# Optimization experiments

Hardware: AMD Instinct MI355X
Metric: run time of the kernel (lower is better)

The kernel has to match this reference:

```python
import jax, jax.numpy as jnp
import numpy as np

N_NODES = 20000
N_EDGES = 320000
NUM_GRAPHS = 64
IN_DIM = 256


def setup_inputs() -> dict:
    key = jax.random.key(0)
    ks = jax.random.split(key, 12)
    x = jax.random.normal(ks[0], (N_NODES, IN_DIM), dtype=jnp.float32)
    edge_index = jax.random.randint(ks[1], (2, N_EDGES), 0, N_NODES, dtype=jnp.int64)
    batch = jnp.sort(jax.random.randint(ks[2], (N_NODES,), 0, NUM_GRAPHS, dtype=jnp.int64))
    def glorot(k, shape):
        lim = float(np.sqrt(6.0 / (shape[0] + shape[1])))
        return jax.random.uniform(k, shape, dtype=jnp.float32, minval=-lim, maxval=lim)
    W1 = glorot(ks[3], (IN_DIM, 256)); b1 = jnp.zeros((256,), jnp.float32)
    W2 = glorot(ks[4], (256, 128));   b2 = jnp.zeros((128,), jnp.float32)
    Wl1 = glorot(ks[5], (128, 64));   bl1 = jnp.zeros((64,), jnp.float32)
    Wl2 = glorot(ks[6], (64, 1));     bl2 = jnp.zeros((1,), jnp.float32)
    return {"x": x, "edge_index": edge_index, "batch": batch,
            "W1": W1, "b1": b1, "W2": W2, "b2": b2,
            "Wl1": Wl1, "bl1": bl1, "Wl2": Wl2, "bl2": bl2}


def gcn_conv(x, src, dst, W, b, n_nodes):
    # PyG GCNConv: add self-loops, symmetric normalization D^-1/2 (A+I) D^-1/2,
    # linear transform first, then gather-scale-scatter aggregation, then bias.
    loop = jnp.arange(n_nodes, dtype=src.dtype)
    s = jnp.concatenate([src, loop])
    d = jnp.concatenate([dst, loop])
    deg = jax.ops.segment_sum(jnp.ones_like(d, dtype=x.dtype), d, num_segments=n_nodes)
    dinv = jnp.where(deg > 0, jax.lax.rsqrt(deg), 0.0)
    norm = dinv[s] * dinv[d]                         # [E+N]
    h = x @ W                                        # [N, out]
    msg = h[s] * norm[:, None]                       # [E+N, out]
    out = jax.ops.segment_sum(msg, d, num_segments=n_nodes)
    return out + b


def global_mean_pool(x, batch, num_graphs):
    sums = jax.ops.segment_sum(x, batch, num_segments=num_graphs)
    cnts = jax.ops.segment_sum(jnp.ones((x.shape[0],), x.dtype), batch, num_segments=num_graphs)
    return sums / jnp.maximum(cnts, 1.0)[:, None]


def reference(x, edge_index, batch, W1, b1, W2, b2, Wl1, bl1, Wl2, bl2):
    n = x.shape[0]
    src, dst = edge_index[0], edge_index[1]
    h = jax.nn.relu(gcn_conv(x, src, dst, W1, b1, n))   # dropout = identity (eval)
    h = jax.nn.relu(gcn_conv(h, src, dst, W2, b2, n))
    g = global_mean_pool(h, batch, NUM_GRAPHS)          # [G, 128]
    g = jax.nn.relu(g @ Wl1 + bl1)
    return jax.nn.sigmoid(g @ Wl2 + bl2)                # [G, 1]
```

## Files before the change

kernel.cpp:

```cpp
#include <hip/hip_runtime.h>
#include <hip/hip_bf16.h>
#include <math.h>

typedef __attribute__((ext_vector_type(8))) short bf16x8;
typedef __attribute__((ext_vector_type(4))) float f32x4;

__device__ __forceinline__ unsigned short f2bf(float f) {
    unsigned int u = __float_as_uint(f);
    unsigned int r = (u + 0x7FFFu + ((u >> 16) & 1u)) >> 16;
    return (unsigned short)r;
}
__device__ __forceinline__ unsigned char f2fp8(float v) {
    int p = __builtin_amdgcn_cvt_pk_fp8_f32(v, v, 0, false);
    return (unsigned char)(p & 0xff);
}
__device__ __forceinline__ unsigned int pk4fp8(float a, float b, float c, float d) {
    int p = __builtin_amdgcn_cvt_pk_fp8_f32(a, b, 0, false);
    p = __builtin_amdgcn_cvt_pk_fp8_f32(c, d, p, true);
    return (unsigned int)p;
}
__device__ __forceinline__ void fp8x8_fma(uint2 u, float w, float* a) {
    a[0] += __builtin_amdgcn_cvt_f32_fp8((int)u.x, 0) * w;
    a[1] += __builtin_amdgcn_cvt_f32_fp8((int)u.x, 1) * w;
    a[2] += __builtin_amdgcn_cvt_f32_fp8((int)u.x, 2) * w;
    a[3] += __builtin_amdgcn_cvt_f32_fp8((int)u.x, 3) * w;
    a[4] += __builtin_amdgcn_cvt_f32_fp8((int)u.y, 0) * w;
    a[5] += __builtin_amdgcn_cvt_f32_fp8((int)u.y, 1) * w;
    a[6] += __builtin_amdgcn_cvt_f32_fp8((int)u.y, 2) * w;
    a[7] += __builtin_amdgcn_cvt_f32_fp8((int)u.y, 3) * w;
}
__device__ __forceinline__ void fp8x4_fma(unsigned int u, float w, float* a) {
    a[0] += __builtin_amdgcn_cvt_f32_fp8((int)u, 0) * w;
    a[1] += __builtin_amdgcn_cvt_f32_fp8((int)u, 1) * w;
    a[2] += __builtin_amdgcn_cvt_f32_fp8((int)u, 2) * w;
    a[3] += __builtin_amdgcn_cvt_f32_fp8((int)u, 3) * w;
}
__device__ __forceinline__ float deg_dinv(int c) { return rsqrtf((float)c + 1.0f); }

__device__ __forceinline__ void load_lds16(const unsigned short* g, unsigned short* l) {
    __builtin_amdgcn_global_load_lds(
        (const __attribute__((address_space(1))) unsigned int*)g,
        (__attribute__((address_space(3))) unsigned int*)l, 16, 0, 0);
}

__global__ __launch_bounds__(256) void prep_kernel(const float* __restrict__ x,
                                                   unsigned short* __restrict__ xh,
                                                   const int* __restrict__ batch,
                                                   int* __restrict__ gstart,
                                                   const float* __restrict__ W1,
                                                   unsigned short* __restrict__ w1t,
                                                   const float* __restrict__ W2,
                                                   unsigned short* __restrict__ w2t,
                                                   int N, int G, int CXB, int BNB) {
    int b = blockIdx.x;
    int tid = threadIdx.x;
    if (b < CXB) {
        size_t idx0 = ((size_t)b * 256 + tid) * 2;
        size_t total4 = (size_t)N * 64;
#pragma unroll
        for (int r = 0; r < 2; r++) {
            size_t idx = idx0 + r;
            if (idx < total4) {
                float4 v = ((const float4*)x)[idx];
                ushort4 o;
                o.x = f2bf(v.x); o.y = f2bf(v.y); o.z = f2bf(v.z); o.w = f2bf(v.w);
                ((ushort4*)xh)[idx] = o;
            }
        }
        return;
    }
    b -= CXB;
    if (b < BNB) {
        int i = b * 256 + tid;
        if (i >= N) return;
        int bb = batch[i];
        if (i == 0) { for (int g = 0; g <= bb; g++) gstart[g] = 0; }
        else { int bp = batch[i - 1]; for (int g = bp + 1; g <= bb; g++) gstart[g] = i; }
        if (i == N - 1) { for (int g = bb + 1; g <= G; g++) gstart[g] = N; }
        return;
    }
    b -= BNB;
    {
        int idx = b * 256 + tid;
        if (idx < 256 * 256) {
            int m = idx >> 8, k = idx & 255;
            w1t[idx] = f2bf(W1[(size_t)k * 256 + m]);
        } else if (idx < 256 * 256 + 128 * 256) {
            int j = idx - 256 * 256;
            int m = j >> 8, k = j & 255;
            w2t[j] = f2bf(W2[(size_t)k * 128 + m]);
        }
    }
}

__device__ __forceinline__ void gemm_body(const unsigned short* __restrict__ A,
                                          const unsigned short* __restrict__ Bt,
                                          unsigned char* __restrict__ C8,
                                          int N, int M, int bx, int by,
                                          unsigned short* As, unsigned short* Bs) {
    const int K = 256;
    int tid = threadIdx.x;
    int wave = tid >> 6, lane = tid & 63;
    int quad = lane >> 4, m16 = lane & 15;
    int r0 = by * 128, c0 = bx * 64;
    int srow = lane >> 2;
    int skoff = (lane & 3) * 8;

    f32x4 acc[2][4];
#pragma unroll
    for (int rg = 0; rg < 2; rg++)
#pragma unroll
        for (int ct = 0; ct < 4; ct++) acc[rg][ct] = (f32x4){0.f, 0.f, 0.f, 0.f};

    for (int kb = 0; kb < K; kb += 32) {
#pragma unroll
        for (int i = 0; i < 2; i++) {
            int brow = wave * 32 + i * 16 + srow;
            int grow = r0 + brow; if (grow >= N) grow = N - 1;
            load_lds16(A + (size_t)grow * K + kb + skoff, As + (wave * 32 + i * 16) * 32);
        }
        {
            int bcol = wave * 16 + srow;
            load_lds16(Bt + (size_t)(c0 + bcol) * K + kb + skoff, Bs + (wave * 16) * 32);
        }
        __syncthreads();
        bf16x8 af[2], bf[4];
#pragma unroll
        for (int rg = 0; rg < 2; rg++)
            af[rg] = *(const bf16x8*)(As + (wave * 32 + rg * 16 + m16) * 32 + quad * 8);
#pragma unroll
        for (int ct = 0; ct < 4; ct++)
            bf[ct] = *(const bf16x8*)(Bs + (ct * 16 + m16) * 32 + quad * 8);
#pragma unroll
        for (int rg = 0; rg < 2; rg++)
#pragma unroll
            for (int ct = 0; ct < 4; ct++)
                acc[rg][ct] = __builtin_amdgcn_mfma_f32_16x16x32_bf16(af[rg], bf[ct], acc[rg][ct], 0, 0, 0);
        __syncthreads();
    }
#pragma unroll
    for (int rg = 0; rg < 2; rg++) {
#pragma unroll
        for (int ct = 0; ct < 4; ct++) {
            int col = c0 + ct * 16 + m16;
#pragma unroll
            for (int r = 0; r < 4; r++) {
                int row = r0 + wave * 32 + rg * 16 + quad * 4 + r;
                if (row < N) C8[(size_t)row * M + col] = f2fp8(acc[rg][ct][r]);
            }
        }
    }
}

__global__ __launch_bounds__(256) void fill_gemm1_kernel(const int* __restrict__ src,
                                                         const int* __restrict__ dst,
                                                         int* __restrict__ cnt,
                                                         int* __restrict__ csr,
                                                         const unsigned short* __restrict__ A,
                                                         const unsigned short* __restrict__ Bt,
                                                         unsigned char* __restrict__ C8,
                                                         int N, int E, int FB) {
    __shared__ unsigned short As[128 * 32];
    __shared__ unsigned short Bs[64 * 32];
    if ((int)blockIdx.x < FB) {
        int e = (blockIdx.x * 256 + threadIdx.x) * 4;
        if (e + 3 < E) {
            int4 d4 = *(const int4*)(dst + e);
            int4 s4 = *(const int4*)(src + e);
            int sl;
            sl = atomicAdd(&cnt[d4.x], 1); if (sl < 64) csr[(d4.x << 6) + sl] = s4.x;
            sl = atomicAdd(&cnt[d4.y], 1); if (sl < 64) csr[(d4.y << 6) + sl] = s4.y;
            sl = atomicAdd(&cnt[d4.z], 1); if (sl < 64) csr[(d4.z << 6) + sl] = s4.z;
            sl = atomicAdd(&cnt[d4.w], 1); if (sl < 64) csr[(d4.w << 6) + sl] = s4.w;
        } else {
            for (; e < E; e++) {
                int d = dst[e];
                int slot = atomicAdd(&cnt[d], 1);
                if (slot < 64) csr[(d << 6) + slot] = src[e];
            }
        }
        return;
    }
    int gb = blockIdx.x - FB;
    gemm_body(A, Bt, C8, N, 256, gb & 3, gb >> 2, As, Bs);
}

__global__ __launch_bounds__(256) void gemm2_kernel(const unsigned short* __restrict__ A,
                                                    const unsigned short* __restrict__ Bt,
                                                    unsigned char* __restrict__ C8, int N) {
    __shared__ unsigned short As[128 * 32];
    __shared__ unsigned short Bs[64 * 32];
    gemm_body(A, Bt, C8, N, 128, blockIdx.x, blockIdx.y, As, Bs);
}

__global__ __launch_bounds__(256) void gather256_kernel(const unsigned char* __restrict__ h8,
                                                        const int* __restrict__ csr,
                                                        const int* __restrict__ cnt,
                                                        const float* __restrict__ bias,
                                                        unsigned short* __restrict__ out, int N) {
    int node = blockIdx.x * 4 + (threadIdx.x >> 6);
    if (node >= N) return;
    int lane = threadIdx.x & 63;
    int half = lane >> 5, hl = lane & 31;
    int beg = node << 6;
    int c = cnt[node]; if (c > 64) c = 64;
    int end = beg + c;
    float a[8] = {0, 0, 0, 0, 0, 0, 0, 0};
    int j = beg;
    for (; j + 7 < end; j += 8) {
        int s0 = csr[j + half], s1 = csr[j + 2 + half];
        int s2 = csr[j + 4 + half], s3 = csr[j + 6 + half];
        float w0 = deg_dinv(cnt[s0]), w1 = deg_dinv(cnt[s1]);
        float w2 = deg_dinv(cnt[s2]), w3 = deg_dinv(cnt[s3]);
        uint2 u0 = *(const uint2*)(h8 + (size_t)s0 * 256 + hl * 8);
        uint2 u1 = *(const uint2*)(h8 + (size_t)s1 * 256 + hl * 8);
        uint2 u2 = *(const uint2*)(h8 + (size_t)s2 * 256 + hl * 8);
        uint2 u3 = *(const uint2*)(h8 + (size_t)s3 * 256 + hl * 8);
        fp8x8_fma(u0, w0, a); fp8x8_fma(u1, w1, a);
        fp8x8_fma(u2, w2, a); fp8x8_fma(u3, w3, a);
    }
    for (; j + 1 < end; j += 2) {
        int s0 = csr[j + half];
        float w0 = deg_dinv(cnt[s0]);
        uint2 u0 = *(const uint2*)(h8 + (size_t)s0 * 256 + hl * 8);
        fp8x8_fma(u0, w0, a);
    }
    if (j < end && half == 0) {
        int s0 = csr[j];
        float w0 = deg_dinv(cnt[s0]);
        uint2 u0 = *(const uint2*)(h8 + (size_t)s0 * 256 + hl * 8);
        fp8x8_fma(u0, w0, a);
    }
#pragma unroll
    for (int i = 0; i < 8; i++) a[i] += __shfl_down(a[i], 32);
    if (half == 0) {
        float dd = deg_dinv(c);
        float self[8] = {0, 0, 0, 0, 0, 0, 0, 0};
        uint2 uh = *(const uint2*)(h8 + (size_t)node * 256 + hl * 8);
        fp8x8_fma(uh, dd, self);
        float4 bv0 = ((const float4*)bias)[hl * 2];
        float4 bv1 = ((const float4*)bias)[hl * 2 + 1];
        float bvf[8] = {bv0.x, bv0.y, bv0.z, bv0.w, bv1.x, bv1.y, bv1.z, bv1.w};
        bf16x8 o;
#pragma unroll
        for (int i = 0; i < 8; i++)
            o[i] = (short)f2bf(fmaxf((a[i] + self[i]) * dd + bvf[i], 0.f));
        ((bf16x8*)(out + (size_t)node * 256))[hl] = o;
    }
}

__global__ __launch_bounds__(256) void gather128_kernel(const unsigned char* __restrict__ t8,
                                                        const int* __restrict__ csr,
                                                        const int* __restrict__ cnt,
                                                        const float* __restrict__ bias,
                                                        unsigned char* __restrict__ out2, int N) {
    int node = blockIdx.x * 4 + (threadIdx.x >> 6);
    if (node >= N) return;
    int lane = threadIdx.x & 63;
    int half = lane >> 5, hl = lane & 31;
    int beg = node << 6;
    int c = cnt[node]; if (c > 64) c = 64;
    int end = beg + c;
    float a[4] = {0, 0, 0, 0};
    int j = beg;
    for (; j + 7 < end; j += 8) {
        int s0 = csr[j + half], s1 = csr[j + 2 + half];
        int s2 = csr[j + 4 + half], s3 = csr[j + 6 + half];
        float w0 = deg_dinv(cnt[s0]), w1 = deg_dinv(cnt[s1]);
        float w2 = deg_dinv(cnt[s2]), w3 = deg_dinv(cnt[s3]);
        unsigned int u0 = *(const unsigned int*)(t8 + (size_t)s0 * 128 + hl * 4);
        unsigned int u1 = *(const unsigned int*)(t8 + (size_t)s1 * 128 + hl * 4);
        unsigned int u2 = *(const unsigned int*)(t8 + (size_t)s2 * 128 + hl * 4);
        unsigned int u3 = *(const unsigned int*)(t8 + (size_t)s3 * 128 + hl * 4);
        fp8x4_fma(u0, w0, a); fp8x4_fma(u1, w1, a);
        fp8x4_fma(u2, w2, a); fp8x4_fma(u3, w3, a);
    }
    for (; j + 1 < end; j += 2) {
        int s0 = csr[j + half];
        float w0 = deg_dinv(cnt[s0]);
        unsigned int u0 = *(const unsigned int*)(t8 + (size_t)s0 * 128 + hl * 4);
        fp8x4_fma(u0, w0, a);
    }
    if (j < end && half == 0) {
        int s0 = csr[j];
        float w0 = deg_dinv(cnt[s0]);
        unsigned int u0 = *(const unsigned int*)(t8 + (size_t)s0 * 128 + hl * 4);
        fp8x4_fma(u0, w0, a);
    }
#pragma unroll
    for (int i = 0; i < 4; i++) a[i] += __shfl_down(a[i], 32);
    if (half == 0) {
        float dd = deg_dinv(c);
        float self[4] = {0, 0, 0, 0};
        unsigned int uh = *(const unsigned int*)(t8 + (size_t)node * 128 + hl * 4);
        fp8x4_fma(uh, dd, self);
        float4 bv = ((const float4*)bias)[hl];
        float r0 = fmaxf((a[0] + self[0]) * dd + bv.x, 0.f);
        float r1 = fmaxf((a[1] + self[1]) * dd + bv.y, 0.f);
        float r2 = fmaxf((a[2] + self[2]) * dd + bv.z, 0.f);
        float r3 = fmaxf((a[3] + self[3]) * dd + bv.w, 0.f);
        ((unsigned int*)(out2 + (size_t)node * 128))[hl] = pk4fp8(r0, r1, r2, r3);
    }
}

__global__ __launch_bounds__(256) void poolhead_kernel(const unsigned char* __restrict__ out2,
                                                       const int* __restrict__ gstart,
                                                       float* __restrict__ gsum,
                                                       int* __restrict__ gdone,
                                                       const float* __restrict__ Wl1,
                                                       const float* __restrict__ bl1,
                                                       const float* __restrict__ Wl2,
                                                       const float* __restrict__ bl2,
                                                       float* __restrict__ out) {
    int g = blockIdx.x >> 3, slice = blockIdx.x & 7;
    int tid = threadIdx.x;
    int hw = tid >> 5, hl = tid & 31;
    int gs = gstart[g], ge = gstart[g + 1];
    float a[4] = {0, 0, 0, 0};
    for (int i = gs + slice * 8 + hw; i < ge; i += 64) {
        unsigned int u = ((const unsigned int*)(out2 + (size_t)i * 128))[hl];
        fp8x4_fma(u, 1.0f, a);
    }
    __shared__ float red[8][128];
#pragma unroll
    for (int k = 0; k < 4; k++) red[hw][hl * 4 + k] = a[k];
    __syncthreads();
    if (tid < 128) {
        float s = 0.f;
#pragma unroll
        for (int w = 0; w < 8; w++) s += red[w][tid];
        if (s != 0.f) atomicAdd(&gsum[g * 128 + tid], s);
    }
    __syncthreads();
    __shared__ int lastflag;
    if (tid == 0) {
        __threadfence();
        int old = atomicAdd(&gdone[g], 1);
        lastflag = (old == 7) ? 1 : 0;
    }
    __syncthreads();
    if (!lastflag) return;
    __shared__ float gv[128];
    if (tid < 128) {
        float s = atomicAdd(&gsum[g * 128 + tid], 0.0f);
        float cntf = fmaxf((float)(ge - gs), 1.0f);
        gv[tid] = s / cntf;
    }
    __syncthreads();
    if (tid < 64) {
        float acc = bl1[tid];
#pragma unroll 8
        for (int k = 0; k < 128; k++) acc += gv[k] * Wl1[k * 64 + tid];
        acc = fmaxf(acc, 0.f);
        float p = acc * Wl2[tid];
#pragma unroll
        for (int off = 32; off; off >>= 1) p += __shfl_down(p, off);
        if (tid == 0) out[g] = 1.f / (1.f + expf(-(p + bl2[0])));
    }
}

extern "C" void kernel_launch(void* const* d_in, const int* in_sizes, int n_in,
                              void* d_out, int out_size, void* d_ws, size_t ws_size,
                              hipStream_t stream) {
    const float* x   = (const float*)d_in[0];
    const int* ei    = (const int*)d_in[1];
    const int* batch = (const int*)d_in[2];
    const float* W1  = (const float*)d_in[3];
    const float* b1  = (const float*)d_in[4];
    const float* W2  = (const float*)d_in[5];
    const float* b2  = (const float*)d_in[6];
    const float* Wl1 = (const float*)d_in[7];
    const float* bl1 = (const float*)d_in[8];
    const float* Wl2 = (const float*)d_in[9];
    const float* bl2 = (const float*)d_in[10];
    float* out = (float*)d_out;

    const int N = in_sizes[2];
    const int E = in_sizes[1] / 2;
    const int G = 64;
    const int* src = ei;
    const int* dst = ei + E;

    char* base = (char*)d_ws;
    size_t off = 0;
    auto carve = [&](size_t bytes) -> char* {
        char* p = base + off;
        off = (off + bytes + 15) & ~(size_t)15;
        return p;
    };
    int*   cnt    = (int*)carve((size_t)N * 4);
    float* gsum   = (float*)carve((size_t)G * 128 * 4);
    int*   gdone  = (int*)carve((size_t)G * 4);
    size_t zero_bytes = (size_t)(N + G * 128 + G) * 4 + 32;
    int*   csr    = (int*)carve((size_t)N * 64 * 4);
    int*   gstart = (int*)carve((size_t)(G + 1) * 4);
    unsigned short* w1t = (unsigned short*)carve((size_t)256 * 256 * 2);
    unsigned short* w2t = (unsigned short*)carve((size_t)128 * 256 * 2);
    unsigned short* xh  = (unsigned short*)carve((size_t)N * 256 * 2);
    unsigned char*  h8  = (unsigned char*)carve((size_t)N * 256);
    unsigned short* o1h = (unsigned short*)carve((size_t)N * 256 * 2);
    unsigned char* t8   = (unsigned char*)xh;
    unsigned char* out2 = h8;

    hipMemsetAsync(d_ws, 0, zero_bytes, stream);

    const int CXB = (int)(((size_t)N * 32 + 255) / 256);
    const int BNB = (N + 255) / 256;
    const int CWB = (256 * 256 + 128 * 256 + 255) / 256;
    prep_kernel<<<CXB + BNB + CWB, 256, 0, stream>>>(
        x, xh, batch, gstart, W1, w1t, W2, w2t, N, G, CXB, BNB);

    const int FB  = (E / 4 + 255) / 256;
    const int GB1 = 4 * ((N + 127) / 128);
    fill_gemm1_kernel<<<FB + GB1, 256, 0, stream>>>(src, dst, cnt, csr,
                                                    xh, w1t, h8, N, E, FB);

    gather256_kernel<<<(N + 3) / 4, 256, 0, stream>>>(h8, csr, cnt, b1, o1h, N);

    {
        dim3 grid(2, (N + 127) / 128);
        gemm2_kernel<<<grid, 256, 0, stream>>>(o1h, w2t, t8, N);
    }
    gather128_kernel<<<(N + 3) / 4, 256, 0, stream>>>(t8, csr, cnt, b2, out2, N);

    poolhead_kernel<<<G * 8, 256, 0, stream>>>(out2, gstart, gsum, gdone,
                                               Wl1, bl1, Wl2, bl2, out);
}
```

Baseline: 173.5 us.

## Fuse layer-2 gather with mean pooling and head; zero workspace inside prep kernel

The second aggregation kernel now accumulates each node's ReLU output directly into per-graph sums with float atomics. The last wave to finish a graph, detected via a per-graph counter, computes the MLP head and sigmoid. The separate pooling kernel, the fp8 intermediate buffer and the memset are removed, and zeroing moves into extra blocks of the prep kernel. This saves launches and a round trip through memory, at the cost of heavy atomic contention on the per-graph sum addresses.

```diff
diff --git a/kernel.cpp b/kernel.cpp
--- a/kernel.cpp
+++ b/kernel.cpp
@@ -13,11 +13,6 @@
 __device__ __forceinline__ unsigned char f2fp8(float v) {
     int p = __builtin_amdgcn_cvt_pk_fp8_f32(v, v, 0, false);
     return (unsigned char)(p & 0xff);
-}
-__device__ __forceinline__ unsigned int pk4fp8(float a, float b, float c, float d) {
-    int p = __builtin_amdgcn_cvt_pk_fp8_f32(a, b, 0, false);
-    p = __builtin_amdgcn_cvt_pk_fp8_f32(c, d, p, true);
-    return (unsigned int)p;
 }
 __device__ __forceinline__ void fp8x8_fma(uint2 u, float w, float* a) {
     a[0] += __builtin_amdgcn_cvt_f32_fp8((int)u.x, 0) * w;
@@ -43,7 +38,8 @@
         (__attribute__((address_space(3))) unsigned int*)l, 16, 0, 0);
 }
 
-__global__ __launch_bounds__(256) void prep_kernel(const float* __restrict__ x,
+__global__ __launch_bounds__(256) void prep_kernel(int* __restrict__ zbase, int zints,
+                                                   const float* __restrict__ x,
                                                    unsigned short* __restrict__ xh,
                                                    const int* __restrict__ batch,
                                                    int* __restrict__ gstart,
@@ -51,9 +47,20 @@
                                                    unsigned short* __restrict__ w1t,
                                                    const float* __restrict__ W2,
                                                    unsigned short* __restrict__ w2t,
-                                                   int N, int G, int CXB, int BNB) {
+                                                   int N, int G,
+                                                   int ZB, int CXB, int BNB) {
     int b = blockIdx.x;
     int tid = threadIdx.x;
+    if (b < ZB) {
+        int i4 = (b * 256 + tid) * 4;
+        if (i4 + 3 < zints) {
+            *(int4*)(zbase + i4) = (int4){0, 0, 0, 0};
+        } else {
+            for (; i4 < zints; i4++) zbase[i4] = 0;
+        }
+        return;
+    }
+    b -= ZB;
     if (b < CXB) {
         size_t idx0 = ((size_t)b * 256 + tid) * 2;
         size_t total4 = (size_t)N * 64;
@@ -249,11 +256,20 @@
     }
 }
 
-__global__ __launch_bounds__(256) void gather128_kernel(const unsigned char* __restrict__ t8,
-                                                        const int* __restrict__ csr,
-                                                        const int* __restrict__ cnt,
-                                                        const float* __restrict__ bias,
-                                                        unsigned char* __restrict__ out2, int N) {
+__global__ __launch_bounds__(256) void gather128_poolhead_kernel(
+        const unsigned char* __restrict__ t8,
+        const int* __restrict__ csr,
+        const int* __restrict__ cnt,
+        const float* __restrict__ bias,
+        const int* __restrict__ batch,
+        const int* __restrict__ gstart,
+        float* __restrict__ gsum,
+        int* __restrict__ gdone,
+        const float* __restrict__ Wl1,
+        const float* __restrict__ bl1,
+        const float* __restrict__ Wl2,
+        const float* __restrict__ bl2,
+        float* __restrict__ out, int N) {
     int node = blockIdx.x * 4 + (threadIdx.x >> 6);
     if (node >= N) return;
     int lane = threadIdx.x & 63;
@@ -289,6 +305,7 @@
     }
 #pragma unroll
     for (int i = 0; i < 4; i++) a[i] += __shfl_down(a[i], 32);
+    int g = batch[node];
     if (half == 0) {
         float dd = deg_dinv(c);
         float self[4] = {0, 0, 0, 0};
@@ -299,64 +316,32 @@
         float r1 = fmaxf((a[1] + self[1]) * dd + bv.y, 0.f);
         float r2 = fmaxf((a[2] + self[2]) * dd + bv.z, 0.f);
         float r3 = fmaxf((a[3] + self[3]) * dd + bv.w, 0.f);
-        ((unsigned int*)(out2 + (size_t)node * 128))[hl] = pk4fp8(r0, r1, r2, r3);
-    }
-}
-
-__global__ __launch_bounds__(256) void poolhead_kernel(const unsigned char* __restrict__ out2,
-                                                       const int* __restrict__ gstart,
-                                                       float* __restrict__ gsum,
-                                                       int* __restrict__ gdone,
-                                                       const float* __restrict__ Wl1,
-                                                       const float* __restrict__ bl1,
-                                                       const float* __restrict__ Wl2,
-                                                       const float* __restrict__ bl2,
-                                                       float* __restrict__ out) {
-    int g = blockIdx.x >> 3, slice = blockIdx.x & 7;
-    int tid = threadIdx.x;
-    int hw = tid >> 5, hl = tid & 31;
-    int gs = gstart[g], ge = gstart[g + 1];
-    float a[4] = {0, 0, 0, 0};
-    for (int i = gs + slice * 8 + hw; i < ge; i += 64) {
-        unsigned int u = ((const unsigned int*)(out2 + (size_t)i * 128))[hl];
-        fp8x4_fma(u, 1.0f, a);
-    }
-    __shared__ float red[8][128];
-#pragma unroll
-    for (int k = 0; k < 4; k++) red[hw][hl * 4 + k] = a[k];
-    __syncthreads();
-    if (tid < 128) {
-        float s = 0.f;
-#pragma unroll
-        for (int w = 0; w < 8; w++) s += red[w][tid];
-        if (s != 0.f) atomicAdd(&gsum[g * 128 + tid], s);
-    }
-    __syncthreads();
-    __shared__ int lastflag;
-    if (tid == 0) {
-        __threadfence();
-        int old = atomicAdd(&gdone[g], 1);
-        lastflag = (old == 7) ? 1 : 0;
-    }
-    __syncthreads();
-    if (!lastflag) return;
-    __shared__ float gv[128];
-    if (tid < 128) {
-        float s = atomicAdd(&gsum[g * 128 + tid], 0.0f);
-        float cntf = fmaxf((float)(ge - gs), 1.0f);
-        gv[tid] = s / cntf;
-    }
-    __syncthreads();
-    if (tid < 64) {
-        float acc = bl1[tid];
+        float* gp = gsum + g * 128 + hl * 4;
+        if (r0 != 0.f) atomicAdd(gp + 0, r0);
+        if (r1 != 0.f) atomicAdd(gp + 1, r1);
+        if (r2 != 0.f) atomicAdd(gp + 2, r2);
+        if (r3 != 0.f) atomicAdd(gp + 3, r3);
+    }
+    __threadfence();
+    int nodecnt = gstart[g + 1] - gstart[g];
+    int done = 0;
+    if (lane == 0) done = atomicAdd(&gdone[g], 1) + 1;
+    done = __shfl(done, 0);
+    if (done != nodecnt) return;
+    float inv = 1.0f / fmaxf((float)nodecnt, 1.0f);
+    float gv0 = atomicAdd(&gsum[g * 128 + lane], 0.0f) * inv;
+    float gv1 = atomicAdd(&gsum[g * 128 + 64 + lane], 0.0f) * inv;
+    float acc = bl1[lane];
 #pragma unroll 8
-        for (int k = 0; k < 128; k++) acc += gv[k] * Wl1[k * 64 + tid];
-        acc = fmaxf(acc, 0.f);
-        float p = acc * Wl2[tid];
-#pragma unroll
-        for (int off = 32; off; off >>= 1) p += __shfl_down(p, off);
-        if (tid == 0) out[g] = 1.f / (1.f + expf(-(p + bl2[0])));
-    }
+    for (int k = 0; k < 64; k++) {
+        acc += __shfl(gv0, k) * Wl1[k * 64 + lane];
+        acc += __shfl(gv1, k) * Wl1[(64 + k) * 64 + lane];
+    }
+    acc = fmaxf(acc, 0.f);
+    float p = acc * Wl2[lane];
+#pragma unroll
+    for (int off = 32; off; off >>= 1) p += __shfl_down(p, off);
+    if (lane == 0) out[g] = 1.f / (1.f + expf(-(p + bl2[0])));
 }
 
 extern "C" void kernel_launch(void* const* d_in, const int* in_sizes, int n_in,
@@ -391,7 +376,7 @@
     int*   cnt    = (int*)carve((size_t)N * 4);
     float* gsum   = (float*)carve((size_t)G * 128 * 4);
     int*   gdone  = (int*)carve((size_t)G * 4);
-    size_t zero_bytes = (size_t)(N + G * 128 + G) * 4 + 32;
+    const int zints = (int)(((char*)(gdone + G) - (char*)d_ws + 3) / 4);
     int*   csr    = (int*)carve((size_t)N * 64 * 4);
     int*   gstart = (int*)carve((size_t)(G + 1) * 4);
     unsigned short* w1t = (unsigned short*)carve((size_t)256 * 256 * 2);
@@ -399,16 +384,14 @@
     unsigned short* xh  = (unsigned short*)carve((size_t)N * 256 * 2);
     unsigned char*  h8  = (unsigned char*)carve((size_t)N * 256);
     unsigned short* o1h = (unsigned short*)carve((size_t)N * 256 * 2);
-    unsigned char* t8   = (unsigned char*)xh;
-    unsigned char* out2 = h8;
-
-    hipMemsetAsync(d_ws, 0, zero_bytes, stream);
-
+    unsigned char*  t8  = (unsigned char*)xh;
+
+    const int ZB  = (zints / 4 + 255) / 256;
     const int CXB = (int)(((size_t)N * 32 + 255) / 256);
     const int BNB = (N + 255) / 256;
     const int CWB = (256 * 256 + 128 * 256 + 255) / 256;
-    prep_kernel<<<CXB + BNB + CWB, 256, 0, stream>>>(
-        x, xh, batch, gstart, W1, w1t, W2, w2t, N, G, CXB, BNB);
+    prep_kernel<<<ZB + CXB + BNB + CWB, 256, 0, stream>>>(
+        (int*)d_ws, zints, x, xh, batch, gstart, W1, w1t, W2, w2t, N, G, ZB, CXB, BNB);
 
     const int FB  = (E / 4 + 255) / 256;
     const int GB1 = 4 * ((N + 127) / 128);
@@ -421,8 +404,7 @@
         dim3 grid(2, (N + 127) / 128);
         gemm2_kernel<<<grid, 256, 0, stream>>>(o1h, w2t, t8, N);
     }
-    gather128_kernel<<<(N + 3) / 4, 256, 0, stream>>>(t8, csr, cnt, b2, out2, N);
-
-    poolhead_kernel<<<G * 8, 256, 0, stream>>>(out2, gstart, gsum, gdone,
-                                               Wl1, bl1, Wl2, bl2, out);
-}
+
+    gather128_poolhead_kernel<<<(N + 3) / 4, 256, 0, stream>>>(
+        t8, csr, cnt, b2, batch, gstart, gsum, gdone, Wl1, bl1, Wl2, bl2, out, N);
+}
```

Measured after the change: 513.3 us. 196% more time.
